# Optimization experiments

Measured on AMD Instinct MI355X. Metric: run time of the kernel, lower is better.

## Reference

```python
import jax, jax.numpy as jnp
import numpy as np

B, S, H = 2, 2048, 1024
NH = 16
HD = H // NH


def setup_inputs() -> dict:
    key = jax.random.key(0)
    ks = jax.random.split(key, 9)
    std = 1.0 / np.sqrt(H)
    inp = {"x": jax.random.normal(ks[0], (B, S, H), dtype=jnp.float32)}
    names = ["Wq", "Wk", "Wv", "Wo"]
    for i, n in enumerate(names):
        inp[n] = jax.random.uniform(ks[1 + i], (H, H), dtype=jnp.float32, minval=-std, maxval=std)
        inp["b" + n[1:]] = jax.random.uniform(ks[5 + i], (H,), dtype=jnp.float32, minval=-std, maxval=std)
    return inp


def reference(x, Wq, Wk, Wv, Wo, bq, bk, bv, bo):
    scale = HD ** -0.5
    # projections: torch Linear is x @ W.T + b
    def proj(W, b):
        y = jnp.einsum('bsh,oh->bso', x, W) + b
        return y.reshape(B, S, NH, HD).transpose(0, 2, 1, 3)  # [B, NH, S, HD]
    Q = proj(Wq, bq)
    K = proj(Wk, bk)
    V = proj(Wv, bv)
    scores = jnp.einsum('bhqd,bhkd->bhqk', Q, K) * scale  # [B, NH, S, S]
    attn = jax.nn.softmax(scores, axis=-1)
    ctx = jnp.einsum('bhqk,bhkd->bhqd', attn, V)
    ctx = ctx.transpose(0, 2, 1, 3).reshape(B, S, H)
    out = jnp.einsum('bsh,oh->bso', ctx, Wo) + bo
    avg_attention = attn.mean(axis=1).mean(axis=1)  # [B, S] (mean over heads, then query dim)
    return out, avg_attention
```

## Files before the change

kernel.cpp:

```cpp
#include <hip/hip_runtime.h>
#include <hip/hip_bf16.h>

#define B_  2
#define S_  2048
#define H_  1024
#define NH_ 16
#define HD_ 64
#define NTOK (B_*S_)

typedef __attribute__((ext_vector_type(8))) short bf16x8;
typedef __attribute__((ext_vector_type(4))) float f32x4;

#define SC2 0.18033688011112042f
#define AVGINV (1.f/((float)NH_*(float)S_))

static __device__ __forceinline__ ushort f2bf(float f) {
    __hip_bfloat16 h = __float2bfloat16(f);
    return *reinterpret_cast<ushort*>(&h);
}
static __device__ __forceinline__ uint cvt_pk_bf16(float lo, float hi) {
    uint r;
    asm("v_cvt_pk_bf16_f32 %0, %1, %2" : "=v"(r) : "v"(lo), "v"(hi));
    return r;
}

static __device__ __forceinline__ void gload_lds16(const void* g, void* l) {
    __builtin_amdgcn_global_load_lds(
        (const __attribute__((address_space(1))) void*)g,
        (__attribute__((address_space(3))) void*)l,
        16, 0, 0);
}

struct PrepArgs {
    const float* src[5];
    ushort*      dst[5];
    float*       zero;
};

static __device__ __forceinline__ void conv8(const float* __restrict__ s,
                                             ushort* __restrict__ d, int i)
{
    const float4 a = reinterpret_cast<const float4*>(s)[2*i + 0];
    const float4 b = reinterpret_cast<const float4*>(s)[2*i + 1];
    ushort u[8];
    u[0] = f2bf(a.x); u[1] = f2bf(a.y); u[2] = f2bf(a.z); u[3] = f2bf(a.w);
    u[4] = f2bf(b.x); u[5] = f2bf(b.y); u[6] = f2bf(b.z); u[7] = f2bf(b.w);
    reinterpret_cast<uint4*>(d)[i] = *reinterpret_cast<uint4*>(u);
}

__global__ __launch_bounds__(256) void prep(PrepArgs a)
{
    int bid = blockIdx.x;
    const int t = threadIdx.x;
    if (bid < 2048) {
        conv8(a.src[0], a.dst[0], bid*256 + t);
        return;
    }
    bid -= 2048;
    if (bid < 2048) {
        const int wi = 1 + (bid >> 9);
        const int i  = (bid & 511)*256 + t;
        conv8(a.src[wi], a.dst[wi], i);
        return;
    }
    bid -= 2048;
    const int i = bid*256 + t;
    if (i < NTOK) a.zero[i] = 0.f;
}

struct GemmArgs {
    const ushort* W[3];
    const float*  bias[3];
    void*         Y[3];
    float         scale[3];
    ushort*       Vt;
};

__global__ __launch_bounds__(256) void gemm_qkv(
    const ushort* __restrict__ A, GemmArgs args, int M, int N, int K)
{
    constexpr int MREP = 4;
    constexpr int BM = MREP * 32;
    __shared__ __align__(16) ushort As[BM * 64];
    __shared__ __align__(16) ushort Bs[128 * 64];

    const int z = blockIdx.z;
    const ushort* __restrict__ W   = args.W[z];
    const float*  __restrict__ bia = args.bias[z];
    const float sc = args.scale[z];

    const int t  = threadIdx.x;
    const int w  = t >> 6;
    const int l  = t & 63;
    const int lq = l >> 4;
    const int ln = l & 15;
    const int wr = w >> 1;
    const int wc = w & 1;
    const int m0 = blockIdx.x * BM;
    const int n0 = blockIdx.y * 128;
    const int srow = l >> 3;
    const int scol = (l & 7) * 8;

    f32x4 acc[MREP][4];
#pragma unroll
    for (int m = 0; m < MREP; ++m)
#pragma unroll
        for (int n = 0; n < 4; ++n) acc[m][n] = f32x4{0.f, 0.f, 0.f, 0.f};

    for (int k0 = 0; k0 < K; k0 += 64) {
        __syncthreads();
#pragma unroll
        for (int i = 0; i < BM/32; ++i) {
            const int rb = i*32 + w*8;
            gload_lds16(A + (size_t)(m0 + rb + srow)*K + k0 + scol, &As[rb*64]);
        }
#pragma unroll
        for (int i = 0; i < 4; ++i) {
            const int rb = i*32 + w*8;
            gload_lds16(W + (size_t)(n0 + rb + srow)*K + k0 + scol, &Bs[rb*64]);
        }
        __syncthreads();
#pragma unroll
        for (int ks = 0; ks < 2; ++ks) {
            bf16x8 bfr[4];
#pragma unroll
            for (int n = 0; n < 4; ++n)
                bfr[n] = *reinterpret_cast<const bf16x8*>(&Bs[(wc*64 + n*16 + ln)*64 + ks*32 + lq*8]);
#pragma unroll
            for (int m = 0; m < MREP; ++m) {
                const bf16x8 afr = *reinterpret_cast<const bf16x8*>(&As[(wr*MREP*16 + m*16 + ln)*64 + ks*32 + lq*8]);
#pragma unroll
                for (int n = 0; n < 4; ++n)
                    acc[m][n] = __builtin_amdgcn_mfma_f32_16x16x32_bf16(afr, bfr[n], acc[m][n], 0, 0, 0);
            }
        }
    }

    float bv[4];
#pragma unroll
    for (int n = 0; n < 4; ++n) bv[n] = bia[n0 + wc*64 + n*16 + ln];

    if (z != 2) {
        ushort* Y = (ushort*)args.Y[z];
#pragma unroll
        for (int m = 0; m < MREP; ++m) {
#pragma unroll
            for (int r = 0; r < 4; ++r) {
                const size_t row = (size_t)(m0 + wr*MREP*16 + m*16 + lq*4 + r);
#pragma unroll
                for (int n = 0; n < 4; ++n) {
                    const int col = n0 + wc*64 + n*16 + ln;
                    Y[row*N + col] = f2bf((acc[m][n][r] + bv[n]) * sc);
                }
            }
        }
    } else {
        const int b = m0 >> 11;
#pragma unroll
        for (int m = 0; m < MREP; ++m) {
            const int s_base = (m0 & 2047) + wr*MREP*16 + m*16 + lq*4;
#pragma unroll
            for (int n = 0; n < 4; ++n) {
                const int col = n0 + wc*64 + n*16 + ln;
                const int h = col >> 6;
                const int d = col & 63;
                ushort4 u;
                u.x = f2bf(acc[m][n][0] + bv[n]);
                u.y = f2bf(acc[m][n][1] + bv[n]);
                u.z = f2bf(acc[m][n][2] + bv[n]);
                u.w = f2bf(acc[m][n][3] + bv[n]);
                *reinterpret_cast<ushort4*>(
                    args.Vt + ((size_t)((b*NH_ + h)*HD_ + d))*S_ + s_base) = u;
            }
        }
    }
}

__global__ __launch_bounds__(256, 2) void attn_pv(
    const ushort* __restrict__ Qb, const ushort* __restrict__ Kb,
    const ushort* __restrict__ Vtg, ushort* __restrict__ ctx,
    float* __restrict__ il2_g)
{
    __shared__ __align__(16) ushort Ks0[64*64];
    __shared__ __align__(16) ushort Ks1[64*64];
    __shared__ __align__(16) ushort Vs0[64*64];
    __shared__ __align__(16) ushort Vs1[64*64];
    __shared__ __align__(16) ushort Ps[4][32*64];

    const int id  = blockIdx.x;
    const int qt_ = (id >> 3) & 15;
    const int bh  = (id & 7) + ((id >> 7) << 3);
    const int b   = bh >> 4;
    const int h   = bh & 15;
    const int q0  = qt_ * 128;

    const int t  = threadIdx.x;
    const int w  = t >> 6;
    const int l  = t & 63;
    const int lq = l >> 4;
    const int ln = l & 15;
    const int ln7 = ln & 7;

    bf16x8 qf[2][2];
#pragma unroll
    for (int qs = 0; qs < 2; ++qs) {
        const ushort* qrow = Qb + ((size_t)(b*S_ + q0 + w*32 + qs*16 + ln))*H_ + h*HD_ + lq*8;
        qf[qs][0] = *reinterpret_cast<const bf16x8*>(qrow);
        qf[qs][1] = *reinterpret_cast<const bf16x8*>(qrow + 32);
    }

    bf16x8 onesb;
#pragma unroll
    for (int j = 0; j < 8; ++j) onesb[j] = (short)0x3F80;

    const f32x4 ZED = f32x4{0.f, 0.f, 0.f, 0.f};

    size_t koff[2], voff[2];
    int    dsto[2];
#pragma unroll
    for (int i = 0; i < 2; ++i) {
        const int chunk = i*256 + t;
        const int row   = chunk >> 3;
        const int c8    = (chunk & 7) ^ (row & 7);
        koff[i] = (size_t)(b*S_ + row)*H_ + h*HD_ + c8*8;
        voff[i] = ((size_t)((b*NH_ + h)*HD_ + row))*S_ + c8*8;
        dsto[i] = chunk*8;
    }

    f32x4 lsacc[2] = {ZED, ZED};
    f32x4 oacc[2][4];
#pragma unroll
    for (int qs = 0; qs < 2; ++qs)
#pragma unroll
        for (int nt = 0; nt < 4; ++nt) oacc[qs][nt] = ZED;

    auto tile_body = [&](const ushort* __restrict__ ksb, const ushort* __restrict__ vsb,
                         int pre_kt, bool do_pre,
                         ushort* __restrict__ kdst, ushort* __restrict__ vdst) {
        if (do_pre) {
#pragma unroll
            for (int i = 0; i < 2; ++i) {
                gload_lds16(Kb + koff[i] + (size_t)pre_kt*H_, &kdst[dsto[i]]);
                gload_lds16(Vtg + voff[i] + pre_kt, &vdst[dsto[i]]);
            }
        }

        f32x4 sacc[2][4];
        {
            bf16x8 kb[4];
#pragma unroll
            for (int nt = 0; nt < 4; ++nt)
                kb[nt] = *reinterpret_cast<const bf16x8*>(
                    &ksb[(nt*16 + ln)*64 + ((lq ^ ln7) * 8)]);
#pragma unroll
            for (int qs = 0; qs < 2; ++qs)
#pragma unroll
                for (int nt = 0; nt < 4; ++nt)
                    sacc[qs][nt] = __builtin_amdgcn_mfma_f32_16x16x32_bf16(
                        kb[nt], qf[qs][0], ZED, 0, 0, 0);
        }
        {
            bf16x8 kb[4];
#pragma unroll
            for (int nt = 0; nt < 4; ++nt)
                kb[nt] = *reinterpret_cast<const bf16x8*>(
                    &ksb[(nt*16 + ln)*64 + (((4 + lq) ^ ln7) * 8)]);
#pragma unroll
            for (int qs = 0; qs < 2; ++qs)
#pragma unroll
                for (int nt = 0; nt < 4; ++nt)
                    sacc[qs][nt] = __builtin_amdgcn_mfma_f32_16x16x32_bf16(
                        kb[nt], qf[qs][1], sacc[qs][nt], 0, 0, 0);
        }

#pragma unroll
        for (int qs = 0; qs < 2; ++qs) {
#pragma unroll
            for (int nt = 0; nt < 4; ++nt) {
                const float e0 = exp2f(sacc[qs][nt][0]);
                const float e1 = exp2f(sacc[qs][nt][1]);
                const float e2 = exp2f(sacc[qs][nt][2]);
                const float e3 = exp2f(sacc[qs][nt][3]);
                uint2 pk;
                pk.x = cvt_pk_bf16(e0, e1);
                pk.y = cvt_pk_bf16(e2, e3);
                const int wch = (nt*2 + (lq >> 1)) ^ ln7;
                *reinterpret_cast<uint2*>(
                    &Ps[w][(qs*16 + ln)*64 + wch*8 + (lq & 1)*4]) = pk;
            }
        }

#pragma unroll
        for (int ks = 0; ks < 2; ++ks) {
            bf16x8 pa[2];
#pragma unroll
            for (int qs = 0; qs < 2; ++qs) {
                pa[qs] = *reinterpret_cast<const bf16x8*>(
                    &Ps[w][(qs*16 + ln)*64 + (((ks*4 + lq) ^ ln7) * 8)]);
                lsacc[qs] = __builtin_amdgcn_mfma_f32_16x16x32_bf16(
                    pa[qs], onesb, lsacc[qs], 0, 0, 0);
            }
#pragma unroll
            for (int nt = 0; nt < 4; ++nt) {
                const bf16x8 vb8 = *reinterpret_cast<const bf16x8*>(
                    &vsb[(nt*16 + ln)*64 + (((ks*4 + lq) ^ ln7) * 8)]);
#pragma unroll
                for (int qs = 0; qs < 2; ++qs)
                    oacc[qs][nt] = __builtin_amdgcn_mfma_f32_16x16x32_bf16(
                        pa[qs], vb8, oacc[qs][nt], 0, 0, 0);
            }
        }

        __syncthreads();
    };

#pragma unroll
    for (int i = 0; i < 2; ++i) {
        gload_lds16(Kb + koff[i], &Ks0[dsto[i]]);
        gload_lds16(Vtg + voff[i], &Vs0[dsto[i]]);
    }
    __syncthreads();

    for (int kt = 0; kt < S_; kt += 128) {
        tile_body(Ks0, Vs0, kt + 64, true, Ks1, Vs1);
        tile_body(Ks1, Vs1, kt + 128, kt + 128 < S_, Ks0, Vs0);
    }

#pragma unroll
    for (int qs = 0; qs < 2; ++qs) {
        float ivr[4];
#pragma unroll
        for (int r = 0; r < 4; ++r) ivr[r] = 1.f / lsacc[qs][r];

        if (ln == 0) {
            float4 o;
            o.x = -__log2f(lsacc[qs][0]);
            o.y = -__log2f(lsacc[qs][1]);
            o.z = -__log2f(lsacc[qs][2]);
            o.w = -__log2f(lsacc[qs][3]);
            *reinterpret_cast<float4*>(
                il2_g + (size_t)(b*NH_ + h)*S_ + q0 + w*32 + qs*16 + lq*4) = o;
        }

        ushort* crow = ctx + ((size_t)(b*S_ + q0 + w*32 + qs*16 + lq*4))*H_ + h*HD_ + ln;
#pragma unroll
        for (int r = 0; r < 4; ++r)
#pragma unroll
            for (int nt = 0; nt < 4; ++nt)
                crow[(size_t)r*H_ + nt*16] = f2bf(oacc[qs][nt][r] * ivr[r]);
    }
}

struct FusedArgs {
    const ushort* Qb; const ushort* Kb;
    const float*  il2; float* avg_out;
    const ushort* A;  const ushort* W;
    const float*  bias; float* Y;
};

__global__ __launch_bounds__(256) void colsum_outproj(FusedArgs fa)
{
    __shared__ __align__(16) char smem[40960];
    const int id = blockIdx.x;
    const int t  = threadIdx.x;
    const int w  = t >> 6;
    const int l  = t & 63;
    const int lq = l >> 4;
    const int ln = l & 15;
    const int ln7 = ln & 7;
    const f32x4 ZED = f32x4{0.f, 0.f, 0.f, 0.f};

    if (id < 512) {
        ushort* KsT = (ushort*)smem;
        ushort* Qs0 = (ushort*)(smem + 16384);
        ushort* Qs1 = (ushort*)(smem + 24576);
        float*  iv  = (float*)(smem + 32768);

        const int kt_ = (id >> 3) & 15;
        const int bh  = (id & 7) + ((id >> 7) << 3);
        const int b   = bh >> 4;
        const int h   = bh & 15;
        const int k0  = kt_ * 128;

        int crow_[2], cc8[2], dsto[2];
#pragma unroll
        for (int i = 0; i < 2; ++i) {
            const int chunk = i*256 + t;
            crow_[i] = chunk >> 3;
            cc8[i]   = (chunk & 7) ^ (crow_[i] & 7);
            dsto[i]  = chunk*8;
        }

#pragma unroll
        for (int i = 0; i < 4; ++i) {
            const int chunk = i*256 + t;
            const int row   = chunk >> 3;
            const int c8    = (chunk & 7) ^ (row & 7);
            gload_lds16(fa.Kb + (size_t)(b*S_ + k0 + row)*H_ + h*HD_ + c8*8, &KsT[chunk*8]);
        }
#pragma unroll
        for (int i = 0; i < 2; ++i) {
            gload_lds16(fa.il2 + (size_t)bh*S_ + (i*256 + t)*4, &iv[(i*256 + t)*4]);
            gload_lds16(fa.Qb + (size_t)(b*S_ + crow_[i])*H_ + h*HD_ + cc8[i]*8, &Qs0[dsto[i]]);
        }
        __syncthreads();

        bf16x8 kf[2][2];
#pragma unroll
        for (int sub = 0; sub < 2; ++sub)
#pragma unroll
            for (int ks = 0; ks < 2; ++ks)
                kf[sub][ks] = *reinterpret_cast<const bf16x8*>(
                    &KsT[(w*32 + sub*16 + ln)*64 + (((ks*4 + lq) ^ ln7) * 8)]);

        float cs4[2][4] = {{0.f,0.f,0.f,0.f},{0.f,0.f,0.f,0.f}};

        for (int qt = 0; qt < S_; qt += 128) {
#pragma unroll
            for (int i = 0; i < 2; ++i)
                gload_lds16(fa.Qb + (size_t)(b*S_ + qt + 64 + crow_[i])*H_ + h*HD_ + cc8[i]*8,
                            &Qs1[dsto[i]]);
#pragma unroll
            for (int c = 0; c < 4; ++c) {
                const bf16x8 a0 = *reinterpret_cast<const bf16x8*>(
                    &Qs0[(c*16 + ln)*64 + ((lq ^ ln7) * 8)]);
                const bf16x8 a1 = *reinterpret_cast<const bf16x8*>(
                    &Qs0[(c*16 + ln)*64 + (((4 + lq) ^ ln7) * 8)]);
                const f32x4 iv4 = *reinterpret_cast<const f32x4*>(&iv[qt + c*16 + lq*4]);
#pragma unroll
                for (int sub = 0; sub < 2; ++sub) {
                    f32x4 sacc = __builtin_amdgcn_mfma_f32_16x16x32_bf16(a0, kf[sub][0], ZED, 0, 0, 0);
                    sacc = __builtin_amdgcn_mfma_f32_16x16x32_bf16(a1, kf[sub][1], sacc, 0, 0, 0);
#pragma unroll
                    for (int r = 0; r < 4; ++r)
                        cs4[sub][r] += exp2f(sacc[r] + iv4[r]);
                }
            }
            __syncthreads();

            if (qt + 128 < S_) {
#pragma unroll
                for (int i = 0; i < 2; ++i)
                    gload_lds16(fa.Qb + (size_t)(b*S_ + qt + 128 + crow_[i])*H_ + h*HD_ + cc8[i]*8,
                                &Qs0[dsto[i]]);
            }
#pragma unroll
            for (int c = 0; c < 4; ++c) {
                const bf16x8 a0 = *reinterpret_cast<const bf16x8*>(
                    &Qs1[(c*16 + ln)*64 + ((lq ^ ln7) * 8)]);
                const bf16x8 a1 = *reinterpret_cast<const bf16x8*>(
                    &Qs1[(c*16 + ln)*64 + (((4 + lq) ^ ln7) * 8)]);
                const f32x4 iv4 = *reinterpret_cast<const f32x4*>(&iv[qt + 64 + c*16 + lq*4]);
#pragma unroll
                for (int sub = 0; sub < 2; ++sub) {
                    f32x4 sacc = __builtin_amdgcn_mfma_f32_16x16x32_bf16(a0, kf[sub][0], ZED, 0, 0, 0);
                    sacc = __builtin_amdgcn_mfma_f32_16x16x32_bf16(a1, kf[sub][1], sacc, 0, 0, 0);
#pragma unroll
                    for (int r = 0; r < 4; ++r)
                        cs4[sub][r] += exp2f(sacc[r] + iv4[r]);
                }
            }
            __syncthreads();
        }

#pragma unroll
        for (int sub = 0; sub < 2; ++sub) {
            float cs = (cs4[sub][0] + cs4[sub][1]) + (cs4[sub][2] + cs4[sub][3]);
            cs += __shfl_xor(cs, 16);
            cs += __shfl_xor(cs, 32);
            if (l < 16)
                atomicAdd(&fa.avg_out[(size_t)b*S_ + k0 + w*32 + sub*16 + l], cs * AVGINV);
        }
    } else {
        ushort* As = (ushort*)smem;
        ushort* Bs = (ushort*)(smem + 8192);

        const int g  = id - 512;
        const int m0 = (g & 63) * 64;
        const int n0 = (g >> 6) * 128;
        const int wr = w >> 1;
        const int wc = w & 1;
        const int srow = l >> 3;
        const int scol = (l & 7) * 8;

        f32x4 acc[2][4];
#pragma unroll
        for (int m = 0; m < 2; ++m)
#pragma unroll
            for (int n = 0; n < 4; ++n) acc[m][n] = ZED;

        for (int k0 = 0; k0 < H_; k0 += 64) {
            __syncthreads();
#pragma unroll
            for (int i = 0; i < 2; ++i) {
                const int rb = i*32 + w*8;
                gload_lds16(fa.A + (size_t)(m0 + rb + srow)*H_ + k0 + scol, &As[rb*64]);
            }
#pragma unroll
            for (int i = 0; i < 4; ++i) {
                const int rb = i*32 + w*8;
                gload_lds16(fa.W + (size_t)(n0 + rb + srow)*H_ + k0 + scol, &Bs[rb*64]);
            }
            __syncthreads();
#pragma unroll
            for (int ks = 0; ks < 2; ++ks) {
                bf16x8 bfr[4];
#pragma unroll
                for (int n = 0; n < 4; ++n)
                    bfr[n] = *reinterpret_cast<const bf16x8*>(&Bs[(wc*64 + n*16 + ln)*64 + ks*32 + lq*8]);
#pragma unroll
                for (int m = 0; m < 2; ++m) {
                    const bf16x8 afr = *reinterpret_cast<const bf16x8*>(&As[(wr*32 + m*16 + ln)*64 + ks*32 + lq*8]);
#pragma unroll
                    for (int n = 0; n < 4; ++n)
                        acc[m][n] = __builtin_amdgcn_mfma_f32_16x16x32_bf16(afr, bfr[n], acc[m][n], 0, 0, 0);
                }
            }
        }

        float bv[4];
#pragma unroll
        for (int n = 0; n < 4; ++n) bv[n] = fa.bias[n0 + wc*64 + n*16 + ln];

#pragma unroll
        for (int m = 0; m < 2; ++m) {
#pragma unroll
            for (int r = 0; r < 4; ++r) {
                const size_t row = (size_t)(m0 + wr*32 + m*16 + lq*4 + r);
#pragma unroll
                for (int n = 0; n < 4; ++n) {
                    const int col = n0 + wc*64 + n*16 + ln;
                    fa.Y[row*H_ + col] = acc[m][n][r] + bv[n];
                }
            }
        }
    }
}

extern "C" void kernel_launch(void* const* d_in, const int* in_sizes, int n_in,
                              void* d_out, int out_size, void* d_ws, size_t ws_size,
                              hipStream_t stream)
{
    const float* x  = (const float*)d_in[0];
    const float* Wq = (const float*)d_in[1];
    const float* bq = (const float*)d_in[2];
    const float* Wk = (const float*)d_in[3];
    const float* bk = (const float*)d_in[4];
    const float* Wv = (const float*)d_in[5];
    const float* bv = (const float*)d_in[6];
    const float* Wo = (const float*)d_in[7];
    const float* bo = (const float*)d_in[8];

    float* out     = (float*)d_out;
    float* avg_out = out + (size_t)NTOK * H_;

    char* ws = (char*)d_ws;
    const size_t mat  = (size_t)NTOK * H_ * sizeof(ushort);
    const size_t wmat = (size_t)H_ * H_ * sizeof(ushort);
    ushort* xb   = (ushort*)(ws);
    ushort* Qb   = (ushort*)(ws + mat);
    ushort* Kb   = (ushort*)(ws + 2*mat);
    ushort* Vtg  = (ushort*)(ws + 3*mat);
    ushort* Wqb  = (ushort*)(ws + 4*mat);
    ushort* Wkb  = (ushort*)(ws + 4*mat + wmat);
    ushort* Wvb  = (ushort*)(ws + 4*mat + 2*wmat);
    ushort* Wob  = (ushort*)(ws + 4*mat + 3*wmat);
    float*  il2  = (float*)(ws + 4*mat + 4*wmat);
    ushort* ctxb = xb;

    const dim3 blk(256);

    {
        PrepArgs pa;
        pa.src[0] = x;  pa.dst[0] = xb;
        pa.src[1] = Wq; pa.dst[1] = Wqb;
        pa.src[2] = Wk; pa.dst[2] = Wkb;
        pa.src[3] = Wv; pa.dst[3] = Wvb;
        pa.src[4] = Wo; pa.dst[4] = Wob;
        pa.zero = avg_out;
        prep<<<dim3(4112), blk, 0, stream>>>(pa);
    }

    {
        GemmArgs ga;
        ga.W[0] = Wqb; ga.W[1] = Wkb; ga.W[2] = Wvb;
        ga.bias[0] = bq; ga.bias[1] = bk; ga.bias[2] = bv;
        ga.Y[0] = Qb; ga.Y[1] = Kb; ga.Y[2] = nullptr;
        ga.scale[0] = SC2; ga.scale[1] = 1.f; ga.scale[2] = 1.f;
        ga.Vt = Vtg;
        gemm_qkv<<<dim3(NTOK/128, H_/128, 3), blk, 0, stream>>>(xb, ga, NTOK, H_, H_);
    }

    attn_pv<<<dim3(512), blk, 0, stream>>>(Qb, Kb, Vtg, ctxb, il2);

    {
        FusedArgs fa;
        fa.Qb = Qb; fa.Kb = Kb; fa.il2 = il2; fa.avg_out = avg_out;
        fa.A = ctxb; fa.W = Wob; fa.bias = bo; fa.Y = out;
        colsum_outproj<<<dim3(1024), blk, 0, stream>>>(fa);
    }
}
```

Before: 166.6 us.

## Split attention over key halves with fp32 partials and separate merge kernel

When the workspace is large enough, the attention kernel splits the key range into two halves, launching twice as many blocks. Each block writes unnormalized fp32 partial outputs and atomically adds its row sums. A new merge kernel adds the partials, normalizes, and writes the bf16 context and log-sum values. This is meant to raise occupancy and parallelism on a 256-CU device, at the cost of extra global traffic, atomics and one more kernel launch. The change also adds MFMA priority hints via s_setprio and drops the launch-bounds occupancy hint.

```diff
diff --git a/kernel.cpp b/kernel.cpp
--- a/kernel.cpp
+++ b/kernel.cpp
@@ -35,6 +35,7 @@
     const float* src[5];
     ushort*      dst[5];
     float*       zero;
+    float*       lzero;
 };
 
 static __device__ __forceinline__ void conv8(const float* __restrict__ s,
@@ -64,8 +65,15 @@
         return;
     }
     bid -= 2048;
-    const int i = bid*256 + t;
-    if (i < NTOK) a.zero[i] = 0.f;
+    if (bid < 16) {
+        const int i = bid*256 + t;
+        if (i < NTOK) a.zero[i] = 0.f;
+        return;
+    }
+    bid -= 16;
+    if (a.lzero) {
+        a.lzero[bid*256 + t] = 0.f;
+    }
 }
 
 struct GemmArgs {
@@ -176,10 +184,12 @@
     }
 }
 
-__global__ __launch_bounds__(256, 2) void attn_pv(
+template<bool SPLIT>
+__global__ __launch_bounds__(256) void attn_pv_t(
     const ushort* __restrict__ Qb, const ushort* __restrict__ Kb,
-    const ushort* __restrict__ Vtg, ushort* __restrict__ ctx,
-    float* __restrict__ il2_g)
+    const ushort* __restrict__ Vtg,
+    ushort* __restrict__ ctx, float* __restrict__ il2_g,
+    float* __restrict__ Opart, float* __restrict__ l_g)
 {
     __shared__ __align__(16) ushort Ks0[64*64];
     __shared__ __align__(16) ushort Ks1[64*64];
@@ -187,12 +197,22 @@
     __shared__ __align__(16) ushort Vs1[64*64];
     __shared__ __align__(16) ushort Ps[4][32*64];
 
-    const int id  = blockIdx.x;
-    const int qt_ = (id >> 3) & 15;
-    const int bh  = (id & 7) + ((id >> 7) << 3);
-    const int b   = bh >> 4;
-    const int h   = bh & 15;
-    const int q0  = qt_ * 128;
+    const int id = blockIdx.x;
+    int qt_, bh, half;
+    if constexpr (SPLIT) {
+        qt_  = (id >> 4) & 15;
+        half = (id >> 3) & 1;
+        bh   = (id & 7) | (((id >> 8) & 3) << 3);
+    } else {
+        qt_  = (id >> 3) & 15;
+        half = 0;
+        bh   = (id & 7) + ((id >> 7) << 3);
+    }
+    const int b  = bh >> 4;
+    const int h  = bh & 15;
+    const int q0 = qt_ * 128;
+    const int kt0 = SPLIT ? half * (S_/2) : 0;
+    const int ktN = SPLIT ? kt0 + (S_/2) : S_;
 
     const int t  = threadIdx.x;
     const int w  = t >> 6;
@@ -246,6 +266,7 @@
         }
 
         f32x4 sacc[2][4];
+        __builtin_amdgcn_s_setprio(1);
         {
             bf16x8 kb[4];
 #pragma unroll
@@ -272,6 +293,7 @@
                     sacc[qs][nt] = __builtin_amdgcn_mfma_f32_16x16x32_bf16(
                         kb[nt], qf[qs][1], sacc[qs][nt], 0, 0, 0);
         }
+        __builtin_amdgcn_s_setprio(0);
 
 #pragma unroll
         for (int qs = 0; qs < 2; ++qs) {
@@ -290,6 +312,7 @@
             }
         }
 
+        __builtin_amdgcn_s_setprio(1);
 #pragma unroll
         for (int ks = 0; ks < 2; ++ks) {
             bf16x8 pa[2];
@@ -310,45 +333,86 @@
                         pa[qs], vb8, oacc[qs][nt], 0, 0, 0);
             }
         }
+        __builtin_amdgcn_s_setprio(0);
 
         __syncthreads();
     };
 
 #pragma unroll
     for (int i = 0; i < 2; ++i) {
-        gload_lds16(Kb + koff[i], &Ks0[dsto[i]]);
-        gload_lds16(Vtg + voff[i], &Vs0[dsto[i]]);
+        gload_lds16(Kb + koff[i] + (size_t)kt0*H_, &Ks0[dsto[i]]);
+        gload_lds16(Vtg + voff[i] + kt0, &Vs0[dsto[i]]);
     }
     __syncthreads();
 
-    for (int kt = 0; kt < S_; kt += 128) {
+    for (int kt = kt0; kt < ktN; kt += 128) {
         tile_body(Ks0, Vs0, kt + 64, true, Ks1, Vs1);
-        tile_body(Ks1, Vs1, kt + 128, kt + 128 < S_, Ks0, Vs0);
-    }
-
-#pragma unroll
-    for (int qs = 0; qs < 2; ++qs) {
-        float ivr[4];
-#pragma unroll
-        for (int r = 0; r < 4; ++r) ivr[r] = 1.f / lsacc[qs][r];
-
-        if (ln == 0) {
-            float4 o;
-            o.x = -__log2f(lsacc[qs][0]);
-            o.y = -__log2f(lsacc[qs][1]);
-            o.z = -__log2f(lsacc[qs][2]);
-            o.w = -__log2f(lsacc[qs][3]);
-            *reinterpret_cast<float4*>(
-                il2_g + (size_t)(b*NH_ + h)*S_ + q0 + w*32 + qs*16 + lq*4) = o;
-        }
-
-        ushort* crow = ctx + ((size_t)(b*S_ + q0 + w*32 + qs*16 + lq*4))*H_ + h*HD_ + ln;
-#pragma unroll
-        for (int r = 0; r < 4; ++r)
-#pragma unroll
-            for (int nt = 0; nt < 4; ++nt)
-                crow[(size_t)r*H_ + nt*16] = f2bf(oacc[qs][nt][r] * ivr[r]);
-    }
+        tile_body(Ks1, Vs1, kt + 128, kt + 128 < ktN, Ks0, Vs0);
+    }
+
+    if constexpr (SPLIT) {
+        float* Op = Opart + (size_t)half * ((size_t)32*S_*64);
+#pragma unroll
+        for (int qs = 0; qs < 2; ++qs) {
+            const int qb = q0 + w*32 + qs*16 + lq*4;
+            if (ln == 0) {
+#pragma unroll
+                for (int r = 0; r < 4; ++r)
+                    atomicAdd(&l_g[(size_t)bh*S_ + qb + r], lsacc[qs][r]);
+            }
+#pragma unroll
+            for (int r = 0; r < 4; ++r) {
+                float* orow = Op + ((size_t)bh*S_ + qb + r)*64 + ln;
+#pragma unroll
+                for (int nt = 0; nt < 4; ++nt)
+                    orow[nt*16] = oacc[qs][nt][r];
+            }
+        }
+    } else {
+#pragma unroll
+        for (int qs = 0; qs < 2; ++qs) {
+            float ivr[4];
+#pragma unroll
+            for (int r = 0; r < 4; ++r) ivr[r] = 1.f / lsacc[qs][r];
+
+            if (ln == 0) {
+                float4 o;
+                o.x = -__log2f(lsacc[qs][0]);
+                o.y = -__log2f(lsacc[qs][1]);
+                o.z = -__log2f(lsacc[qs][2]);
+                o.w = -__log2f(lsacc[qs][3]);
+                *reinterpret_cast<float4*>(
+                    il2_g + (size_t)bh*S_ + q0 + w*32 + qs*16 + lq*4) = o;
+            }
+
+            ushort* crow = ctx + ((size_t)(b*S_ + q0 + w*32 + qs*16 + lq*4))*H_ + h*HD_ + ln;
+#pragma unroll
+            for (int r = 0; r < 4; ++r)
+#pragma unroll
+                for (int nt = 0; nt < 4; ++nt)
+                    crow[(size_t)r*H_ + nt*16] = f2bf(oacc[qs][nt][r] * ivr[r]);
+        }
+    }
+}
+
+__global__ __launch_bounds__(256) void merge_ctx(
+    const float* __restrict__ Opart, const float* __restrict__ l_g,
+    ushort* __restrict__ ctx, float* __restrict__ il2_g)
+{
+    const int t   = threadIdx.x;
+    const int row = blockIdx.x*4 + (t >> 6);
+    const int d   = t & 63;
+    const int bh  = row >> 11;
+    const int q   = row & 2047;
+    const int b   = bh >> 4;
+    const int h   = bh & 15;
+
+    const float lt  = l_g[row];
+    const float inv = 1.f / lt;
+    const size_t hs = (size_t)32*S_*64;
+    const float o = Opart[(size_t)row*64 + d] + Opart[hs + (size_t)row*64 + d];
+    ctx[((size_t)(b*S_ + q))*H_ + h*HD_ + d] = f2bf(o * inv);
+    if (d == 0) il2_g[row] = -__log2f(lt);
 }
 
 struct FusedArgs {
@@ -566,7 +630,12 @@
     ushort* Wvb  = (ushort*)(ws + 4*mat + 2*wmat);
     ushort* Wob  = (ushort*)(ws + 4*mat + 3*wmat);
     float*  il2  = (float*)(ws + 4*mat + 4*wmat);
+    float*  l_g  = (float*)(ws + 4*mat + 4*wmat + 262144);
+    float*  Opart= (float*)(ws + 4*mat + 4*wmat + 524288);
     ushort* ctxb = xb;
+
+    const size_t need_split = 4*mat + 4*wmat + 524288 + (size_t)2*32*S_*64*sizeof(float);
+    const bool use_split = (ws_size >= need_split);
 
     const dim3 blk(256);
 
@@ -577,8 +646,9 @@
         pa.src[2] = Wk; pa.dst[2] = Wkb;
         pa.src[3] = Wv; pa.dst[3] = Wvb;
         pa.src[4] = Wo; pa.dst[4] = Wob;
-        pa.zero = avg_out;
-        prep<<<dim3(4112), blk, 0, stream>>>(pa);
+        pa.zero  = avg_out;
+        pa.lzero = use_split ? l_g : nullptr;
+        prep<<<dim3(use_split ? 4368 : 4112), blk, 0, stream>>>(pa);
     }
 
     {
@@ -591,7 +661,14 @@
         gemm_qkv<<<dim3(NTOK/128, H_/128, 3), blk, 0, stream>>>(xb, ga, NTOK, H_, H_);
     }
 
-    attn_pv<<<dim3(512), blk, 0, stream>>>(Qb, Kb, Vtg, ctxb, il2);
+    if (use_split) {
+        attn_pv_t<true><<<dim3(1024), blk, 0, stream>>>(
+            Qb, Kb, Vtg, nullptr, nullptr, Opart, l_g);
+        merge_ctx<<<dim3(32*S_/4), blk, 0, stream>>>(Opart, l_g, ctxb, il2);
+    } else {
+        attn_pv_t<false><<<dim3(512), blk, 0, stream>>>(
+            Qb, Kb, Vtg, ctxb, il2, nullptr, nullptr);
+    }
 
     {
         FusedArgs fa;
```

After: 182.0 us. +9.3%, slower.
